# Kernel optimization log

Hardware: AMD Instinct MI355X
Metric: run time of the kernel (lower is better)

## Reference

```python
import jax, jax.numpy as jnp
import numpy as np


def setup_inputs() -> dict:
    key = jax.random.key(0)
    k1, k2, k3, k4 = jax.random.split(key, 4)
    d_in, d_out, B, T = 1024, 1024, 4, 2048
    scale = 1.0 / np.sqrt(d_in)
    return {
        "x": jax.random.normal(k1, (B, T, d_in), dtype=jnp.float32),
        "Wq": jax.random.normal(k2, (d_in, d_out), dtype=jnp.float32) * scale,
        "Wk": jax.random.normal(k3, (d_in, d_out), dtype=jnp.float32) * scale,
        "Wv": jax.random.normal(k4, (d_in, d_out), dtype=jnp.float32) * scale,
    }


def reference(x, Wq, Wk, Wv):
    # x: [B, T, d_in]; Wq/Wk/Wv: [d_in, d_out] (Linear, bias=False)
    q = jnp.einsum("btd,de->bte", x, Wq)
    k = jnp.einsum("btd,de->bte", x, Wk)
    v = jnp.einsum("btd,de->bte", x, Wv)
    d_out = k.shape[-1]
    scores = jnp.einsum("bqe,bke->bqk", q, k)  # [B, T, T]
    T = x.shape[1]
    causal = jnp.triu(jnp.ones((T, T), dtype=bool), k=1)  # True above diagonal
    scores = jnp.where(causal[None, :, :], -jnp.inf, scores)
    # original divides after masking; -inf stays -inf so math is identical
    att = jax.nn.softmax(scores / jnp.sqrt(jnp.asarray(d_out, scores.dtype)), axis=-1)
    # dropout p=0.0 -> identity
    return jnp.einsum("bqk,bke->bqe", att, v)
```

## Files before the change

### kernel.cpp

```cpp
#include <hip/hip_runtime.h>
#include <stdint.h>
#include <math.h>

typedef unsigned short u16;
typedef __bf16 bf16x8 __attribute__((ext_vector_type(8)));
typedef float f32x4 __attribute__((ext_vector_type(4)));

enum { M_QKV = 0, M_SCORE = 1, M_PV = 2 };

__device__ __forceinline__ u16 f2bf(float f) {
    union { float f; unsigned int u; } a; a.f = f;
    unsigned int u = a.u;
    u += 0x7FFFu + ((u >> 16) & 1u);
    return (u16)(u >> 16);
}

__device__ __forceinline__ void async_load16(const void* g, void* l) {
    __builtin_amdgcn_global_load_lds(
        (const __attribute__((address_space(1))) void*)g,
        (__attribute__((address_space(3))) void*)l,
        16, 0, 0);
}

template<int MODE, int TBM>
__device__ __forceinline__ void gemm_core(
    const u16* __restrict__ A, const u16* __restrict__ Bt,
    void* __restrict__ Cv, float* __restrict__ rowsum,
    int bm, int bn, int bz, int M, int N, int K, float kfac,
    u16* As, u16* Bs)
{
    constexpr int KB  = 64;
    constexpr int NI  = TBM / 32;
    constexpr int ACH = TBM / 32;
    constexpr int BCH = 4;

    const int tid  = threadIdx.x;
    const int lane = tid & 63;
    const int wv   = tid >> 6;
    const int wm   = wv >> 1;
    const int wn   = wv & 1;

    f32x4 acc[NI][4] = {};

    const int rowA0 = bm * TBM, rowB0 = bn * 128;
    const int lrow  = lane >> 3;
    const int lslot = lane & 7;
    const int sg    = (lslot ^ lrow) * 8;

    int kEnd = K;
    if (MODE == M_PV) { int ke = (bm + 1) * TBM; kEnd = ke < K ? ke : K; }

    const int lm   = lane & 15;
    const int quad = lane >> 4;
    const int rx   = lm & 7;

    for (int k0 = 0; k0 < kEnd; k0 += KB) {
        #pragma unroll
        for (int c = 0; c < ACH; ++c) {
            const int cc  = wv * ACH + c;
            const int row = cc * 8 + lrow;
            async_load16(&A[(size_t)(rowA0 + row) * K + k0 + sg], &As[cc * 512 + lane * 8]);
        }
        #pragma unroll
        for (int c = 0; c < BCH; ++c) {
            const int cc  = wv * BCH + c;
            const int row = cc * 8 + lrow;
            async_load16(&Bt[(size_t)(rowB0 + row) * K + k0 + sg], &Bs[cc * 512 + lane * 8]);
        }
        __syncthreads();

        #pragma unroll
        for (int h = 0; h < 2; ++h) {
            const int sl = (((h * 4 + quad) ^ rx) * 8);
            bf16x8 af[NI], bfr[4];
            #pragma unroll
            for (int i = 0; i < NI; ++i)
                af[i] = *reinterpret_cast<const bf16x8*>(
                    &As[(wm * (TBM / 2) + i * 16 + lm) * KB + sl]);
            #pragma unroll
            for (int j = 0; j < 4; ++j)
                bfr[j] = *reinterpret_cast<const bf16x8*>(
                    &Bs[(wn * 64 + j * 16 + lm) * KB + sl]);
            #pragma unroll
            for (int i = 0; i < NI; ++i)
                #pragma unroll
                for (int j = 0; j < 4; ++j)
                    acc[i][j] = __builtin_amdgcn_mfma_f32_16x16x32_bf16(af[i], bfr[j], acc[i][j], 0, 0, 0);
        }
        __syncthreads();
    }

    if (MODE == M_QKV) {
        u16* C = (u16*)Cv + (size_t)(bn >> 3) * ((size_t)M * 1024);
        #pragma unroll
        for (int i = 0; i < NI; ++i)
            #pragma unroll
            for (int j = 0; j < 4; ++j) {
                const int r0 = rowA0 + wm * (TBM / 2) + i * 16 + quad * 4;
                const int c0 = (rowB0 + wn * 64 + j * 16 + lm) & 1023;
                #pragma unroll
                for (int g = 0; g < 4; ++g)
                    C[(size_t)(r0 + g) * 1024 + c0] = f2bf(acc[i][j][g]);
            }
    } else if (MODE == M_SCORE) {
        u16* E = (u16*)Cv + (size_t)bz * ((size_t)M * N);
        float rs[NI][4];
        #pragma unroll
        for (int i = 0; i < NI; ++i)
            #pragma unroll
            for (int g = 0; g < 4; ++g) rs[i][g] = 0.f;
        #pragma unroll
        for (int i = 0; i < NI; ++i)
            #pragma unroll
            for (int j = 0; j < 4; ++j) {
                const int r0 = rowA0 + wm * (TBM / 2) + i * 16 + quad * 4;
                const int c  = rowB0 + wn * 64 + j * 16 + lm;
                #pragma unroll
                for (int g = 0; g < 4; ++g) {
                    const int r = r0 + g;
                    float e = (c <= r) ? exp2f(acc[i][j][g] * kfac) : 0.f;
                    E[(size_t)r * N + c] = f2bf(e);
                    rs[i][g] += e;
                }
            }
        #pragma unroll
        for (int i = 0; i < NI; ++i)
            #pragma unroll
            for (int g = 0; g < 4; ++g) {
                float v = rs[i][g];
                v += __shfl_xor(v, 1); v += __shfl_xor(v, 2);
                v += __shfl_xor(v, 4); v += __shfl_xor(v, 8);
                rs[i][g] = v;
            }
        if (lm == 0) {
            #pragma unroll
            for (int i = 0; i < NI; ++i)
                #pragma unroll
                for (int g = 0; g < 4; ++g) {
                    const int r = rowA0 + wm * (TBM / 2) + i * 16 + quad * 4 + g;
                    atomicAdd(&rowsum[(size_t)bz * M + r], rs[i][g]);
                }
        }
    } else {
        float* C = (float*)Cv + (size_t)bz * ((size_t)M * N);
        #pragma unroll
        for (int i = 0; i < NI; ++i) {
            const int r0 = rowA0 + wm * (TBM / 2) + i * 16 + quad * 4;
            float inv[4];
            #pragma unroll
            for (int g = 0; g < 4; ++g)
                inv[g] = 1.f / rowsum[(size_t)bz * M + r0 + g];
            #pragma unroll
            for (int j = 0; j < 4; ++j) {
                const int c0 = rowB0 + wn * 64 + j * 16 + lm;
                #pragma unroll
                for (int g = 0; g < 4; ++g)
                    C[(size_t)(r0 + g) * N + c0] = acc[i][j][g] * inv[g];
            }
        }
    }
}

__global__ __launch_bounds__(512, 2)
void k_qkv2(const u16* __restrict__ Xb, const u16* __restrict__ Wt,
            u16* __restrict__ Q, int M, int N, int K)
{
    extern __shared__ __attribute__((aligned(16))) u16 S[];
    const int tid  = threadIdx.x;
    const int lane = tid & 63;
    const int wv   = tid >> 6;
    const int wm   = wv >> 2;
    const int wn   = wv & 3;
    const int bn   = blockIdx.x;
    const int bm   = blockIdx.y;
    const int rowA0 = bm * 128, rowB0 = bn * 256;

    const int lrow  = lane >> 3;
    const int lslot = lane & 7;
    const int sg    = (lslot ^ lrow) * 8;
    const int lm    = lane & 15;
    const int quad  = lane >> 4;
    const int rx    = lm & 7;

    f32x4 acc[4][4] = {};

    const int nt = K >> 6;

    auto stage = [&](int t, int b) {
        u16* As = S + b * 24576;
        u16* Bs = As + 8192;
        const int k0 = t << 6;
        #pragma unroll
        for (int c = 0; c < 2; ++c) {
            const int cc  = wv * 2 + c;
            const int row = cc * 8 + lrow;
            async_load16(&Xb[(size_t)(rowA0 + row) * K + k0 + sg], &As[cc * 512 + lane * 8]);
        }
        #pragma unroll
        for (int c = 0; c < 4; ++c) {
            const int cc  = wv * 4 + c;
            const int row = cc * 8 + lrow;
            async_load16(&Wt[(size_t)(rowB0 + row) * K + k0 + sg], &Bs[cc * 512 + lane * 8]);
        }
    };

    auto compute = [&](int b) {
        const u16* As = S + b * 24576;
        const u16* Bs = As + 8192;
        #pragma unroll
        for (int h = 0; h < 2; ++h) {
            const int sl = (((h * 4 + quad) ^ rx) * 8);
            bf16x8 af[4], bfr[4];
            #pragma unroll
            for (int i = 0; i < 4; ++i)
                af[i] = *reinterpret_cast<const bf16x8*>(
                    &As[(wm * 64 + i * 16 + lm) * 64 + sl]);
            #pragma unroll
            for (int j = 0; j < 4; ++j)
                bfr[j] = *reinterpret_cast<const bf16x8*>(
                    &Bs[(wn * 64 + j * 16 + lm) * 64 + sl]);
            #pragma unroll
            for (int i = 0; i < 4; ++i)
                #pragma unroll
                for (int j = 0; j < 4; ++j)
                    acc[i][j] = __builtin_amdgcn_mfma_f32_16x16x32_bf16(af[i], bfr[j], acc[i][j], 0, 0, 0);
        }
    };

    stage(0, 0);
    stage(1, 1);
    asm volatile("s_waitcnt vmcnt(6)" ::: "memory");
    __builtin_amdgcn_s_barrier();

    int cb = 0;
    #pragma unroll 1
    for (int t = 0; t < nt - 2; ++t) {
        int sb = cb + 2; if (sb >= 3) sb -= 3;
        stage(t + 2, sb);
        compute(cb);
        asm volatile("s_waitcnt vmcnt(6)" ::: "memory");
        __builtin_amdgcn_s_barrier();
        if (++cb == 3) cb = 0;
    }
    compute(cb);
    asm volatile("s_waitcnt vmcnt(0)" ::: "memory");
    __builtin_amdgcn_s_barrier();
    if (++cb == 3) cb = 0;
    compute(cb);

    u16* C = Q + (size_t)(bn >> 2) * ((size_t)M * 1024);
    const int cbase = (rowB0 & 1023) + wn * 64;
    #pragma unroll
    for (int i = 0; i < 4; ++i)
        #pragma unroll
        for (int j = 0; j < 4; ++j) {
            const int r0 = rowA0 + wm * 64 + i * 16 + quad * 4;
            const int c0 = cbase + j * 16 + lm;
            #pragma unroll
            for (int g = 0; g < 4; ++g)
                C[(size_t)(r0 + g) * 1024 + c0] = f2bf(acc[i][j][g]);
        }
}

__global__ __launch_bounds__(256)
void k_score_vt(const u16* __restrict__ Q, const u16* __restrict__ Kb,
                u16* __restrict__ E, float* __restrict__ rowsum,
                const u16* __restrict__ Vb, u16* __restrict__ Vt,
                int T, int D, float kfac, int nTri)
{
    __shared__ __attribute__((aligned(16))) u16 As[128 * 64];
    __shared__ __attribute__((aligned(16))) u16 Bs[128 * 64];
    __shared__ u16 tt[32][33];
    const int bz = blockIdx.z;

    if ((int)blockIdx.x < nTri) {
        const int idx = blockIdx.x;
        int bm = (int)((sqrtf(8.f * (float)idx + 1.f) - 1.f) * 0.5f);
        while (bm * (bm + 1) / 2 > idx) --bm;
        while ((bm + 1) * (bm + 2) / 2 <= idx) ++bm;
        const int bn = idx - bm * (bm + 1) / 2;
        gemm_core<M_SCORE, 128>(Q + (size_t)bz * T * D, Kb + (size_t)bz * T * D,
                                E, rowsum, bm, bn, bz, T, T, D, kfac, As, Bs);
    } else {
        const int t  = blockIdx.x - nTri;
        const int cx = t & 31;
        const int cy = t >> 5;
        const u16* V = Vb + (size_t)bz * T * D;
        u16*      Vo = Vt + (size_t)bz * D * T;
        const int c0 = cx * 32, r0 = cy * 32;
        const int tx = threadIdx.x & 31, ty = threadIdx.x >> 5;
        #pragma unroll
        for (int s = 0; s < 32; s += 8)
            tt[ty + s][tx] = V[(size_t)(r0 + ty + s) * D + c0 + tx];
        __syncthreads();
        #pragma unroll
        for (int s = 0; s < 32; s += 8)
            Vo[(size_t)(c0 + ty + s) * T + r0 + tx] = tt[tx][ty + s];
    }
}

__global__ __launch_bounds__(256)
void k_pv(const u16* __restrict__ E, const u16* __restrict__ Vt,
          float* __restrict__ out, const float* __restrict__ rowsum,
          int T, int D)
{
    __shared__ __attribute__((aligned(16))) u16 As[128 * 64];
    __shared__ __attribute__((aligned(16))) u16 Bs[128 * 64];
    const int bz = blockIdx.z;
    const int bm = (gridDim.y - 1) - blockIdx.y;
    gemm_core<M_PV, 128>(E + (size_t)bz * T * T, Vt + (size_t)bz * D * T,
                         out, (float*)rowsum, bm, blockIdx.x, bz,
                         T, D, T, 0.f, As, Bs);
}

__global__ __launch_bounds__(256)
void k_prep(const float* __restrict__ x,
            const float* __restrict__ W0, const float* __restrict__ W1,
            const float* __restrict__ W2,
            u16* __restrict__ Xb, u16* __restrict__ Wt, float* __restrict__ RS,
            int D, int nCX, int nW)
{
    const int bx = blockIdx.x;
    if (bx < nCX) {
        long long i = ((long long)bx * 256 + threadIdx.x) * 8;
        const float4 a = *(const float4*)(x + i);
        const float4 b = *(const float4*)(x + i + 4);
        union { u16 u[8]; float4 v; } r;
        r.u[0] = f2bf(a.x); r.u[1] = f2bf(a.y); r.u[2] = f2bf(a.z); r.u[3] = f2bf(a.w);
        r.u[4] = f2bf(b.x); r.u[5] = f2bf(b.y); r.u[6] = f2bf(b.z); r.u[7] = f2bf(b.w);
        *(float4*)(Xb + i) = r.v;
    } else if (bx < nCX + nW) {
        __shared__ u16 t[32][33];
        const int w  = bx - nCX;
        const int z  = w >> 10;
        const int rm = w & 1023;
        const float* W = z == 0 ? W0 : (z == 1 ? W1 : W2);
        u16* dst = Wt + (size_t)z * D * D;
        const int c0 = (rm & 31) * 32, r0 = (rm >> 5) * 32;
        const int tx = threadIdx.x & 31, ty = threadIdx.x >> 5;
        #pragma unroll
        for (int s = 0; s < 32; s += 8)
            t[ty + s][tx] = f2bf(W[(size_t)(r0 + ty + s) * D + c0 + tx]);
        __syncthreads();
        #pragma unroll
        for (int s = 0; s < 32; s += 8)
            dst[(size_t)(c0 + ty + s) * D + r0 + tx] = t[tx][ty + s];
    } else {
        const int t = bx - nCX - nW;
        ((float4*)RS)[t * 256 + threadIdx.x] = float4{0.f, 0.f, 0.f, 0.f};
    }
}

extern "C" void kernel_launch(void* const* d_in, const int* in_sizes, int n_in,
                              void* d_out, int out_size, void* d_ws, size_t ws_size,
                              hipStream_t stream)
{
    const int B = 4, T = 2048, D = 1024;
    const float* x  = (const float*)d_in[0];
    const float* Wq = (const float*)d_in[1];
    const float* Wk = (const float*)d_in[2];
    const float* Wv = (const float*)d_in[3];
    float* out = (float*)d_out;

    const size_t nX = (size_t)B * T * D;
    u16* Xb = (u16*)d_ws;
    u16* Wt = Xb + nX;
    u16* Q  = Wt + 3 * (size_t)D * D;
    u16* Kb = Q + nX;
    u16* Vb = Kb + nX;
    u16* Vt = Vb + nX;
    char* rest = (char*)(Vt + nX);
    const size_t fixed   = (size_t)((char*)rest - (char*)d_ws);
    const size_t perb_E  = (size_t)T * T * 2;
    const size_t perb_rs = (size_t)T * 4;
    const bool full = ws_size >= fixed + (size_t)B * (perb_E + perb_rs);
    const int nb = full ? B : 1;
    u16*   E  = (u16*)rest;
    float* RS = (float*)(E + nb * (size_t)T * T);

    const float kfac = 1.4426950408889634f / 32.0f;
    const int nTri128 = 136;
    const int nCX = (int)(nX / (8 * 256));
    const int nW  = 3 * (D / 32) * (D / 32);
    const int nRS = (nb * T) / (4 * 256);

    static bool attr_done = false;
    if (!attr_done) {
        (void)hipFuncSetAttribute((const void*)k_qkv2,
                                  hipFuncAttributeMaxDynamicSharedMemorySize,
                                  147456);
        attr_done = true;
    }

    if (full) {
        k_prep<<<dim3(nCX + nW + nRS), 256, 0, stream>>>(
            x, Wq, Wk, Wv, Xb, Wt, RS, D, nCX, nW);
        k_qkv2<<<dim3(3 * D / 256, (B * T) / 128), 512, 147456, stream>>>(
            Xb, Wt, Q, B * T, 3 * D, D);
        k_score_vt<<<dim3(nTri128 + (D / 32) * (T / 32), 1, B), 256, 0, stream>>>(
            Q, Kb, E, RS, Vb, Vt, T, D, kfac, nTri128);
        k_pv<<<dim3(D / 128, T / 128, B), 256, 0, stream>>>(E, Vt, out, RS, T, D);
    } else {
        k_prep<<<dim3(nCX + nW + nRS), 256, 0, stream>>>(
            x, Wq, Wk, Wv, Xb, Wt, RS, D, nCX, nW);
        k_qkv2<<<dim3(3 * D / 256, (B * T) / 128), 512, 147456, stream>>>(
            Xb, Wt, Q, B * T, 3 * D, D);
        for (int b = 0; b < B; ++b) {
            const size_t ob = (size_t)b * T * D;
            if (b) hipMemsetAsync(RS, 0, (size_t)T * 4, stream);
            k_score_vt<<<dim3(nTri128 + (D / 32) * (T / 32), 1, 1), 256, 0, stream>>>(
                Q + ob, Kb + ob, E, RS, Vb + ob, Vt, T, D, kfac, nTri128);
            k_pv<<<dim3(D / 128, T / 128, 1), 256, 0, stream>>>(
                E, Vt, out + ob, RS, T, D);
        }
    }
}
```

Baseline: 244.4 us.

## Store score exponentials as packed lower-triangular 128x128 tiles reused in PV

Result: no change. 245.5 us (+0.5%).

```diff
diff --git a/kernel.cpp b/kernel.cpp
--- a/kernel.cpp
+++ b/kernel.cpp
@@ -59,7 +59,12 @@
         for (int c = 0; c < ACH; ++c) {
             const int cc  = wv * ACH + c;
             const int row = cc * 8 + lrow;
-            async_load16(&A[(size_t)(rowA0 + row) * K + k0 + sg], &As[cc * 512 + lane * 8]);
+            const u16* src;
+            if (MODE == M_PV)
+                src = &A[(size_t)(k0 >> 7) * 16384 + (size_t)row * 128 + (k0 & 127) + sg];
+            else
+                src = &A[(size_t)(rowA0 + row) * K + k0 + sg];
+            async_load16(src, &As[cc * 512 + lane * 8]);
         }
         #pragma unroll
         for (int c = 0; c < BCH; ++c) {
@@ -90,36 +95,25 @@
         __syncthreads();
     }
 
-    if (MODE == M_QKV) {
-        u16* C = (u16*)Cv + (size_t)(bn >> 3) * ((size_t)M * 1024);
+    if (MODE == M_SCORE) {
+        u16* E = (u16*)Cv;
+        float rs[NI][4];
         #pragma unroll
         for (int i = 0; i < NI; ++i)
             #pragma unroll
+            for (int g = 0; g < 4; ++g) rs[i][g] = 0.f;
+        #pragma unroll
+        for (int i = 0; i < NI; ++i)
+            #pragma unroll
             for (int j = 0; j < 4; ++j) {
-                const int r0 = rowA0 + wm * (TBM / 2) + i * 16 + quad * 4;
-                const int c0 = (rowB0 + wn * 64 + j * 16 + lm) & 1023;
-                #pragma unroll
-                for (int g = 0; g < 4; ++g)
-                    C[(size_t)(r0 + g) * 1024 + c0] = f2bf(acc[i][j][g]);
-            }
-    } else if (MODE == M_SCORE) {
-        u16* E = (u16*)Cv + (size_t)bz * ((size_t)M * N);
-        float rs[NI][4];
-        #pragma unroll
-        for (int i = 0; i < NI; ++i)
-            #pragma unroll
-            for (int g = 0; g < 4; ++g) rs[i][g] = 0.f;
-        #pragma unroll
-        for (int i = 0; i < NI; ++i)
-            #pragma unroll
-            for (int j = 0; j < 4; ++j) {
-                const int r0 = rowA0 + wm * (TBM / 2) + i * 16 + quad * 4;
-                const int c  = rowB0 + wn * 64 + j * 16 + lm;
+                const int rl = wm * (TBM / 2) + i * 16 + quad * 4;
+                const int cl = wn * 64 + j * 16 + lm;
+                const int c  = rowB0 + cl;
                 #pragma unroll
                 for (int g = 0; g < 4; ++g) {
-                    const int r = r0 + g;
+                    const int r = rowA0 + rl + g;
                     float e = (c <= r) ? exp2f(acc[i][j][g] * kfac) : 0.f;
-                    E[(size_t)r * N + c] = f2bf(e);
+                    E[(size_t)(rl + g) * 128 + cl] = f2bf(e);
                     rs[i][g] += e;
                 }
             }
@@ -264,7 +258,7 @@
 
 __global__ __launch_bounds__(256)
 void k_score_vt(const u16* __restrict__ Q, const u16* __restrict__ Kb,
-                u16* __restrict__ E, float* __restrict__ rowsum,
+                u16* __restrict__ Epk, float* __restrict__ rowsum,
                 const u16* __restrict__ Vb, u16* __restrict__ Vt,
                 int T, int D, float kfac, int nTri)
 {
@@ -279,8 +273,9 @@
         while (bm * (bm + 1) / 2 > idx) --bm;
         while ((bm + 1) * (bm + 2) / 2 <= idx) ++bm;
         const int bn = idx - bm * (bm + 1) / 2;
+        u16* Etile = Epk + ((size_t)bz * nTri + idx) * 16384;
         gemm_core<M_SCORE, 128>(Q + (size_t)bz * T * D, Kb + (size_t)bz * T * D,
-                                E, rowsum, bm, bn, bz, T, T, D, kfac, As, Bs);
+                                Etile, rowsum, bm, bn, bz, T, T, D, kfac, As, Bs);
     } else {
         const int t  = blockIdx.x - nTri;
         const int cx = t & 31;
@@ -300,15 +295,16 @@
 }
 
 __global__ __launch_bounds__(256)
-void k_pv(const u16* __restrict__ E, const u16* __restrict__ Vt,
+void k_pv(const u16* __restrict__ Epk, const u16* __restrict__ Vt,
           float* __restrict__ out, const float* __restrict__ rowsum,
-          int T, int D)
+          int T, int D, int nTri)
 {
     __shared__ __attribute__((aligned(16))) u16 As[128 * 64];
     __shared__ __attribute__((aligned(16))) u16 Bs[128 * 64];
     const int bz = blockIdx.z;
     const int bm = (gridDim.y - 1) - blockIdx.y;
-    gemm_core<M_PV, 128>(E + (size_t)bz * T * T, Vt + (size_t)bz * D * T,
+    const u16* Arow = Epk + ((size_t)bz * nTri + (size_t)bm * (bm + 1) / 2) * 16384;
+    gemm_core<M_PV, 128>(Arow, Vt + (size_t)bz * D * T,
                          out, (float*)rowsum, bm, blockIdx.x, bz,
                          T, D, T, 0.f, As, Bs);
 }
@@ -363,26 +359,20 @@
     float* out = (float*)d_out;
 
     const size_t nX = (size_t)B * T * D;
-    u16* Xb = (u16*)d_ws;
-    u16* Wt = Xb + nX;
-    u16* Q  = Wt + 3 * (size_t)D * D;
-    u16* Kb = Q + nX;
-    u16* Vb = Kb + nX;
-    u16* Vt = Vb + nX;
-    char* rest = (char*)(Vt + nX);
-    const size_t fixed   = (size_t)((char*)rest - (char*)d_ws);
-    const size_t perb_E  = (size_t)T * T * 2;
-    const size_t perb_rs = (size_t)T * 4;
-    const bool full = ws_size >= fixed + (size_t)B * (perb_E + perb_rs);
-    const int nb = full ? B : 1;
-    u16*   E  = (u16*)rest;
-    float* RS = (float*)(E + nb * (size_t)T * T);
+    u16* Xb  = (u16*)d_ws;
+    u16* Wt  = Xb + nX;
+    u16* Epk = (u16*)d_ws;
+    u16* Q   = Wt + 3 * (size_t)D * D;
+    u16* Kb  = Q + nX;
+    u16* Vb  = Kb + nX;
+    u16* Vt  = Vb + nX;
+    float* RS = (float*)(Vt + nX);
 
     const float kfac = 1.4426950408889634f / 32.0f;
     const int nTri128 = 136;
     const int nCX = (int)(nX / (8 * 256));
     const int nW  = 3 * (D / 32) * (D / 32);
-    const int nRS = (nb * T) / (4 * 256);
+    const int nRS = (B * T) / (4 * 256);
 
     static bool attr_done = false;
     if (!attr_done) {
@@ -392,26 +382,12 @@
         attr_done = true;
     }
 
-    if (full) {
-        k_prep<<<dim3(nCX + nW + nRS), 256, 0, stream>>>(
-            x, Wq, Wk, Wv, Xb, Wt, RS, D, nCX, nW);
-        k_qkv2<<<dim3(3 * D / 256, (B * T) / 128), 512, 147456, stream>>>(
-            Xb, Wt, Q, B * T, 3 * D, D);
-        k_score_vt<<<dim3(nTri128 + (D / 32) * (T / 32), 1, B), 256, 0, stream>>>(
-            Q, Kb, E, RS, Vb, Vt, T, D, kfac, nTri128);
-        k_pv<<<dim3(D / 128, T / 128, B), 256, 0, stream>>>(E, Vt, out, RS, T, D);
-    } else {
-        k_prep<<<dim3(nCX + nW + nRS), 256, 0, stream>>>(
-            x, Wq, Wk, Wv, Xb, Wt, RS, D, nCX, nW);
-        k_qkv2<<<dim3(3 * D / 256, (B * T) / 128), 512, 147456, stream>>>(
-            Xb, Wt, Q, B * T, 3 * D, D);
-        for (int b = 0; b < B; ++b) {
-            const size_t ob = (size_t)b * T * D;
-            if (b) hipMemsetAsync(RS, 0, (size_t)T * 4, stream);
-            k_score_vt<<<dim3(nTri128 + (D / 32) * (T / 32), 1, 1), 256, 0, stream>>>(
-                Q + ob, Kb + ob, E, RS, Vb + ob, Vt, T, D, kfac, nTri128);
-            k_pv<<<dim3(D / 128, T / 128, 1), 256, 0, stream>>>(
-                E, Vt, out + ob, RS, T, D);
-        }
-    }
-}
+    k_prep<<<dim3(nCX + nW + nRS), 256, 0, stream>>>(
+        x, Wq, Wk, Wv, Xb, Wt, RS, D, nCX, nW);
+    k_qkv2<<<dim3(3 * D / 256, (B * T) / 128), 512, 147456, stream>>>(
+        Xb, Wt, Q, B * T, 3 * D, D);
+    k_score_vt<<<dim3(nTri128 + (D / 32) * (T / 32), 1, B), 256, 0, stream>>>(
+        Q, Kb, Epk, RS, Vb, Vt, T, D, kfac, nTri128);
+    k_pv<<<dim3(D / 128, T / 128, B), 256, 0, stream>>>(
+        Epk, Vt, out, RS, T, D, nTri128);
+}
```
